# Performance work log

Hardware: AMD Instinct MI355X
Metric: run time of the kernel (lower is better)

## Reference

```python
import jax, jax.numpy as jnp
import numpy as np

WS = 11      # window_size
SIGMA = 1.5
CH = 4       # channels / groups (hardcoded in forward)
SCALE = 1.0


def _gaussian_window(dtype):
    x = np.arange(WS, dtype=np.float64) - WS // 2
    g = np.exp(-(x ** 2) / (2.0 * SIGMA ** 2))
    g = g / g.sum()
    w2 = np.outer(g, g).astype(np.float32)          # [WS, WS]
    w = np.broadcast_to(w2, (CH, 1, WS, WS)).copy()  # [O, I/groups, kH, kW]
    return jnp.asarray(w, dtype=dtype)


def _dwconv(x, w):
    # depthwise conv2d, groups=CH, VALID padding (matches F.conv2d default padding=0)
    return jax.lax.conv_general_dilated(
        x, w, window_strides=(1, 1), padding='VALID',
        dimension_numbers=('NCHW', 'OIHW', 'NCHW'),
        feature_group_count=CH)


def setup_inputs() -> dict:
    key = jax.random.key(0)
    k1, k2 = jax.random.split(key)
    X = jax.random.normal(k1, (16, 4, 512, 512), dtype=jnp.float32)
    Y = jax.random.normal(k2, (16, 4, 512, 512), dtype=jnp.float32)
    return {"X": X, "Y": Y}


def reference(X, Y):
    w = _gaussian_window(X.dtype)
    muX = _dwconv(X, w)
    muY = _dwconv(Y, w)
    muX_sq, muY_sq, muXY = muX * muX, muY * muY, muX * muY
    sigmaX_sq = _dwconv(X * X, w) - muX_sq
    sigmaY_sq = _dwconv(Y * Y, w) - muY_sq
    sigmaXY = _dwconv(X * Y, w) - muXY
    C1 = (0.01 * SCALE) ** 2
    C2 = (0.03 * SCALE) ** 2
    v1 = 2.0 * sigmaXY + C2
    v2 = sigmaX_sq + sigmaY_sq + C2
    ssim_map = (2.0 * muXY + C1) * v1 / ((muX_sq + muY_sq + C1) * v2)
    return 1.0 - ssim_map.mean()
```

## Files before the change

### kernel.cpp

```cpp
#include <hip/hip_runtime.h>
#include <hip/hip_bf16.h>
#include <cmath>


#define IMG   512
#define ODIM  502
#define SC    16
#define BR    64
#define WPB   4
#define BC    (SC * WPB)
#define GX    8
#define GY    8
#define NC    64
#define NBLK  (GX * GY * NC)

typedef float          f32x4  __attribute__((ext_vector_type(4)));
typedef __bf16         bf16x8 __attribute__((ext_vector_type(8)));
typedef __bf16         bf16x4 __attribute__((ext_vector_type(4)));
typedef short          s16x4  __attribute__((ext_vector_type(4)));
typedef unsigned int   u32x2  __attribute__((ext_vector_type(2)));
typedef unsigned int   u32x4  __attribute__((ext_vector_type(4)));

union F8 { bf16x8 v; __bf16 b[8]; u32x4 q; };
union F4 { bf16x4 v; s16x4 s; __bf16 b[4]; u32x2 q; };

__device__ __forceinline__ unsigned short bfbits(float f) {
    __bf16 h = (__bf16)f;
    return __builtin_bit_cast(unsigned short, h);
}

__device__ __forceinline__ f32x4 mfma16(const F4& a, const F4& b, f32x4 c) {
    return __builtin_amdgcn_mfma_f32_16x16x16bf16_1k(a.s, b.s, c, 0, 0, 0);
}

struct GaussW { float g[11]; };

__global__ __launch_bounds__(256, 4) void ssim_mfma_kernel(
    const float* __restrict__ X, const float* __restrict__ Y,
    float* __restrict__ partial, GaussW gw)
{
    __shared__ unsigned short wl[16][32];
    __shared__ float wsum[WPB];

    const int tid  = threadIdx.x;
    const int lane = tid & 63;
    const int wave = tid >> 6;
    const int m    = lane & 15;
    const int g    = lane >> 4;

#pragma unroll
    for (int it = 0; it < 2; ++it) {
        const int t  = tid + 256 * it;
        const int mm = t >> 5, kk = t & 31;
        const int d  = kk - mm;
        wl[mm][kk] = bfbits((d >= 0 && d < 11) ? gw.g[d] : 0.f);
    }
    __syncthreads();

    const int gx0 = blockIdx.x * BC + SC * wave;
    const int gy0 = blockIdx.y * BR;
    const int nc  = blockIdx.z;
    const float* __restrict__ Xp = X + (size_t)nc * IMG * IMG;
    const float* __restrict__ Yp = Y + (size_t)nc * IMG * IMG;

    F8 wf;  wf.q  = *(const u32x4*)&wl[m][8 * g];
    F4 wa0; wa0.q = *(const u32x2*)&wl[m][4 * g];
    F4 wa1; wa1.q = *(const u32x2*)&wl[m][16 + 4 * g];
    const f32x4 z = {0.f, 0.f, 0.f, 0.f};

    F4 h[5][5];
    const int cs = min(gx0 + 8 * g, IMG - 8);
#pragma unroll
    for (int rt = 0; rt < 5; ++rt) {
        const int gy = min(gy0 + 16 * rt + m, IMG - 1);
        const float* xr = Xp + gy * IMG + cs;
        const float* yr = Yp + gy * IMG + cs;
        const f32x4 a0 = *(const f32x4*)xr;
        const f32x4 a1 = *(const f32x4*)(xr + 4);
        const f32x4 b0 = *(const f32x4*)yr;
        const f32x4 b1 = *(const f32x4*)(yr + 4);

        F8 fx, fy, fxx, fyy, fxy;
#pragma unroll
        for (int j = 0; j < 4; ++j) {
            fx.b[j]      = (__bf16)a0[j];
            fx.b[4 + j]  = (__bf16)a1[j];
            fy.b[j]      = (__bf16)b0[j];
            fy.b[4 + j]  = (__bf16)b1[j];
            fxx.b[j]     = (__bf16)(a0[j] * a0[j]);
            fxx.b[4 + j] = (__bf16)(a1[j] * a1[j]);
            fyy.b[j]     = (__bf16)(b0[j] * b0[j]);
            fyy.b[4 + j] = (__bf16)(b1[j] * b1[j]);
            fxy.b[j]     = (__bf16)(a0[j] * b0[j]);
            fxy.b[4 + j] = (__bf16)(a1[j] * b1[j]);
        }
        const f32x4 dX  = __builtin_amdgcn_mfma_f32_16x16x32_bf16(fx.v,  wf.v, z, 0, 0, 0);
        const f32x4 dY  = __builtin_amdgcn_mfma_f32_16x16x32_bf16(fy.v,  wf.v, z, 0, 0, 0);
        const f32x4 dXX = __builtin_amdgcn_mfma_f32_16x16x32_bf16(fxx.v, wf.v, z, 0, 0, 0);
        const f32x4 dYY = __builtin_amdgcn_mfma_f32_16x16x32_bf16(fyy.v, wf.v, z, 0, 0, 0);
        const f32x4 dXY = __builtin_amdgcn_mfma_f32_16x16x32_bf16(fxy.v, wf.v, z, 0, 0, 0);
#pragma unroll
        for (int i = 0; i < 4; ++i) {
            h[rt][0].b[i] = (__bf16)dX[i];
            h[rt][1].b[i] = (__bf16)dY[i];
            h[rt][2].b[i] = (__bf16)dXX[i];
            h[rt][3].b[i] = (__bf16)dYY[i];
            h[rt][4].b[i] = (__bf16)dXY[i];
        }
    }

    float acc = 0.f;
#pragma unroll
    for (int vt = 0; vt < 4; ++vt) {
        f32x4 e[5];
#pragma unroll
        for (int q = 0; q < 5; ++q) {
            e[q] = mfma16(wa1, h[vt + 1][q], z);
            e[q] = mfma16(wa0, h[vt][q], e[q]);
        }
        const float C1 = 1e-4f, C2 = 9e-4f;
#pragma unroll
        for (int i = 0; i < 4; ++i) {
            const int gy = gy0 + 16 * vt + 4 * g + i;
            const int gx = gx0 + m;
            const float mX = e[0][i], mY = e[1][i];
            const float muXX = mX * mX;
            const float muYY = mY * mY;
            const float muXY = mX * mY;
            const float sXX = e[2][i] - muXX;
            const float sYY = e[3][i] - muYY;
            const float sXY = e[4][i] - muXY;
            const float num = (2.f * muXY + C1) * (2.f * sXY + C2);
            const float den = (muXX + muYY + C1) * (sXX + sYY + C2);
            const float val = __fdividef(num, den);
            if (gy < ODIM && gx < ODIM) acc += val;
        }
    }

#pragma unroll
    for (int off = 32; off > 0; off >>= 1)
        acc += __shfl_down(acc, off, 64);

    if (lane == 0) wsum[wave] = acc;
    __syncthreads();
    if (tid == 0) {
        const float tsum = (wsum[0] + wsum[1]) + (wsum[2] + wsum[3]);
        partial[((size_t)blockIdx.z * gridDim.y + blockIdx.y) * gridDim.x + blockIdx.x] = tsum;
    }
}

__global__ __launch_bounds__(512) void ssim_finish_kernel(
    const float* __restrict__ partial, float* __restrict__ out)
{
    __shared__ double sd[512];
    const float4* p4 = (const float4*)partial;
    double local = 0.0;
#pragma unroll
    for (int i = 0; i < 2; ++i) {
        const float4 v = p4[threadIdx.x + 512 * i];
        local += ((double)v.x + (double)v.y) + ((double)v.z + (double)v.w);
    }
    sd[threadIdx.x] = local;
    __syncthreads();
    for (int s = 256; s > 0; s >>= 1) {
        if (threadIdx.x < s) sd[threadIdx.x] += sd[threadIdx.x + s];
        __syncthreads();
    }
    if (threadIdx.x == 0) {
        const double cnt = (double)NC * (double)ODIM * (double)ODIM;
        out[0] = (float)(1.0 - sd[0] / cnt);
    }
}

extern "C" void kernel_launch(void* const* d_in, const int* in_sizes, int n_in,
                              void* d_out, int out_size, void* d_ws, size_t ws_size,
                              hipStream_t stream) {
    const float* X = (const float*)d_in[0];
    const float* Y = (const float*)d_in[1];
    float* out = (float*)d_out;
    float* partial = (float*)d_ws;

    GaussW gw;
    {
        double gd[11], s = 0.0;
        for (int i = 0; i < 11; ++i) {
            const double x = (double)(i - 5);
            gd[i] = std::exp(-(x * x) / (2.0 * 1.5 * 1.5));
            s += gd[i];
        }
        for (int i = 0; i < 11; ++i) gw.g[i] = (float)(gd[i] / s);
    }

    dim3 grid(GX, GY, NC);
    ssim_mfma_kernel<<<grid, 256, 0, stream>>>(X, Y, partial, gw);
    ssim_finish_kernel<<<1, 512, 0, stream>>>(partial, out);
}
```

Before: 50.93 us.

## Double the row tile per block and stream horizontal tiles through a rolling buffer

Each block now covers 128 output rows instead of 64, so the halo rows read and horizontally convolved per block drop from 5/4 to 9/8 of the useful rows. The horizontal-pass results are kept in a two-slot rolling buffer instead of a full 5-tile array, which lowers register pressure and lets the launch bound ask for 5 blocks per SM. The weight LDS row is padded to 40 entries, which looks aimed at bank conflicts. The trade is fewer blocks (half the grid) and a longer serial chain of loads per wave, which may expose more memory latency.

```diff
diff --git a/kernel.cpp b/kernel.cpp
--- a/kernel.cpp
+++ b/kernel.cpp
@@ -6,13 +6,14 @@
 #define IMG   512
 #define ODIM  502
 #define SC    16
-#define BR    64
+#define BR    128
 #define WPB   4
 #define BC    (SC * WPB)
 #define GX    8
-#define GY    8
+#define GY    4
 #define NC    64
 #define NBLK  (GX * GY * NC)
+#define NVT   8
 
 typedef float          f32x4  __attribute__((ext_vector_type(4)));
 typedef __bf16         bf16x8 __attribute__((ext_vector_type(8)));
@@ -35,11 +36,11 @@
 
 struct GaussW { float g[11]; };
 
-__global__ __launch_bounds__(256, 4) void ssim_mfma_kernel(
+__global__ __launch_bounds__(256, 5) void ssim_mfma_kernel(
     const float* __restrict__ X, const float* __restrict__ Y,
     float* __restrict__ partial, GaussW gw)
 {
-    __shared__ unsigned short wl[16][32];
+    __shared__ unsigned short wl[16][40];
     __shared__ float wsum[WPB];
 
     const int tid  = threadIdx.x;
@@ -48,12 +49,10 @@
     const int m    = lane & 15;
     const int g    = lane >> 4;
 
-#pragma unroll
-    for (int it = 0; it < 2; ++it) {
-        const int t  = tid + 256 * it;
-        const int mm = t >> 5, kk = t & 31;
+    for (int t = tid; t < 16 * 40; t += 256) {
+        const int mm = t / 40, kk = t - 40 * mm;
         const int d  = kk - mm;
-        wl[mm][kk] = bfbits((d >= 0 && d < 11) ? gw.g[d] : 0.f);
+        wl[mm][kk] = bfbits((kk < 32 && d >= 0 && d < 11) ? gw.g[d] : 0.f);
     }
     __syncthreads();
 
@@ -68,10 +67,9 @@
     F4 wa1; wa1.q = *(const u32x2*)&wl[m][16 + 4 * g];
     const f32x4 z = {0.f, 0.f, 0.f, 0.f};
 
-    F4 h[5][5];
     const int cs = min(gx0 + 8 * g, IMG - 8);
-#pragma unroll
-    for (int rt = 0; rt < 5; ++rt) {
+
+    auto computeH = [&](F4 (&hd)[5], int rt) {
         const int gy = min(gy0 + 16 * rt + m, IMG - 1);
         const float* xr = Xp + gy * IMG + cs;
         const float* yr = Yp + gy * IMG + cs;
@@ -101,22 +99,29 @@
         const f32x4 dXY = __builtin_amdgcn_mfma_f32_16x16x32_bf16(fxy.v, wf.v, z, 0, 0, 0);
 #pragma unroll
         for (int i = 0; i < 4; ++i) {
-            h[rt][0].b[i] = (__bf16)dX[i];
-            h[rt][1].b[i] = (__bf16)dY[i];
-            h[rt][2].b[i] = (__bf16)dXX[i];
-            h[rt][3].b[i] = (__bf16)dYY[i];
-            h[rt][4].b[i] = (__bf16)dXY[i];
+            hd[0].b[i] = (__bf16)dX[i];
+            hd[1].b[i] = (__bf16)dY[i];
+            hd[2].b[i] = (__bf16)dXX[i];
+            hd[3].b[i] = (__bf16)dYY[i];
+            hd[4].b[i] = (__bf16)dXY[i];
         }
-    }
+    };
+
+    F4 hh[2][5];
+    computeH(hh[0], 0);
 
     float acc = 0.f;
 #pragma unroll
-    for (int vt = 0; vt < 4; ++vt) {
+    for (int vt = 0; vt < NVT; ++vt) {
+        computeH(hh[(vt + 1) & 1], vt + 1);
+        const F4 (&h0)[5] = hh[vt & 1];
+        const F4 (&h1)[5] = hh[(vt + 1) & 1];
+
         f32x4 e[5];
 #pragma unroll
         for (int q = 0; q < 5; ++q) {
-            e[q] = mfma16(wa1, h[vt + 1][q], z);
-            e[q] = mfma16(wa0, h[vt][q], e[q]);
+            e[q] = mfma16(wa1, h1[q], z);
+            e[q] = mfma16(wa0, h0[q], e[q]);
         }
         const float C1 = 1e-4f, C2 = 9e-4f;
 #pragma unroll
@@ -154,12 +159,8 @@
 {
     __shared__ double sd[512];
     const float4* p4 = (const float4*)partial;
-    double local = 0.0;
-#pragma unroll
-    for (int i = 0; i < 2; ++i) {
-        const float4 v = p4[threadIdx.x + 512 * i];
-        local += ((double)v.x + (double)v.y) + ((double)v.z + (double)v.w);
-    }
+    const float4 v = p4[threadIdx.x];
+    double local = ((double)v.x + (double)v.y) + ((double)v.z + (double)v.w);
     sd[threadIdx.x] = local;
     __syncthreads();
     for (int s = 256; s > 0; s >>= 1) {
```

Measured after the change: 48.16 us. 5.4% less time.
